# Performance work log

Measured on AMD Instinct MI355X. Metric: run time of the kernel, lower is better.

Reference implementation:

```python
import jax, jax.numpy as jnp
import numpy as np

N, C = 131072, 32          # scene points, raw feature channels
K, L, B1 = 2048, 64, 8     # points per leaf, num leaves, level-1 branching
D_PROJ, D_HID, D = 128, 256, 512


def _lin(key, fan_in, fan_out):
    return jax.random.normal(key, (fan_in, fan_out), jnp.float32) / np.sqrt(fan_in)


def setup_inputs() -> dict:
    key = jax.random.key(0)
    ks = jax.random.split(key, 12)
    coords = jax.random.normal(ks[0], (N, 3), jnp.float32)
    feats = jax.random.normal(ks[1], (N, C), jnp.float32)
    # regular partition of the scene into 64 leaves of 2048 points each
    leaf_indices = jnp.arange(N, dtype=jnp.int32).reshape(L, K)
    leaf_center_idx = jax.random.randint(ks[2], (L,), 0, N, dtype=jnp.int32)
    l1_center_idx = jax.random.randint(ks[3], (B1,), 0, N, dtype=jnp.int32)
    return {
        'coords': coords, 'feats': feats,
        'leaf_indices': leaf_indices,
        'leaf_center_idx': leaf_center_idx,
        'l1_center_idx': l1_center_idx,
        'root_center_idx': 0,
        # projection MLP: C -> 128 -> 128
        'Wp1': _lin(ks[4], C, D_PROJ), 'bp1': jnp.zeros((D_PROJ,), jnp.float32),
        'Wp2': _lin(ks[5], D_PROJ, D_PROJ), 'bp2': jnp.zeros((D_PROJ,), jnp.float32),
        # encoder per-point MLP: (3 + 128) -> 256 -> 512
        'We1': _lin(ks[6], 3 + D_PROJ, D_HID), 'be1': jnp.zeros((D_HID,), jnp.float32),
        'We2': _lin(ks[7], D_HID, D), 'be2': jnp.zeros((D,), jnp.float32),
        # aggregator: (D + 3) -> 512 per child, max-pool, 512 -> 512
        'Wa1': _lin(ks[8], D + 3, D), 'ba1': jnp.zeros((D,), jnp.float32),
        'Wa2': _lin(ks[9], D, D), 'ba2': jnp.zeros((D,), jnp.float32),
    }


def reference(coords, feats, leaf_indices, leaf_center_idx, l1_center_idx,
              root_center_idx, Wp1, bp1, Wp2, bp2, We1, be1, We2, be2,
              Wa1, ba1, Wa2, ba2):
    # ---- leaves: gather + projection + PointNet encoder (batched over all leaves) ----
    pts = coords[leaf_indices]                       # (L, K, 3)
    pf = feats[leaf_indices]                         # (L, K, C)
    centers = coords[leaf_center_idx]                # (L, 3)
    rel = pts - centers[:, None, :]                  # relative coords
    proj = jax.nn.relu(pf @ Wp1 + bp1) @ Wp2 + bp2   # (L, K, D_PROJ)
    x = jnp.concatenate([rel, proj], axis=-1)        # (L, K, 3+D_PROJ)
    h = jax.nn.relu(x @ We1 + be1)                   # (L, K, D_HID)
    point_feats = jax.nn.relu(h @ We2 + be2)         # (L, K, D)
    leaf_feat = point_feats.max(axis=1)              # (L, D) max pool per leaf

    # ---- aggregator with spatial context ----
    def aggregate(child_feats, child_pos, parent_pos):
        r = child_pos - parent_pos[None, :]                       # (M, 3)
        z = jnp.concatenate([child_feats, r], axis=-1)            # (M, D+3)
        g = jax.nn.relu(z @ Wa1 + ba1)                            # (M, D)
        return g.max(axis=0) @ Wa2 + ba2                          # (D,)

    # level 1: each of B1 parents aggregates L//B1 leaf children
    cf = leaf_feat.reshape(B1, L // B1, D)
    cp = centers.reshape(B1, L // B1, 3)
    pp = coords[l1_center_idx]                                    # (B1, 3)
    level1 = jax.vmap(aggregate)(cf, cp, pp)                      # (B1, D)

    # level 0: root aggregates the B1 level-1 features
    root = aggregate(level1, pp, coords[root_center_idx])         # (D,)

    # rows: [level_0 (1), level_1 (B1), level_2 (L)]
    return jnp.concatenate([root[None, :], level1, leaf_feat], axis=0)
```

## Files before the change

kernel.cpp:

```cpp
#include <hip/hip_runtime.h>

#define NPTS   131072
#define CIN    32
#define KPL    2048
#define NLEAF  64
#define NB1    8
#define DPJ    128
#define DHID   256
#define DOUT   512
#define TM     128

typedef __attribute__((ext_vector_type(8))) short  short8;
typedef __attribute__((ext_vector_type(4))) float  f32x4;

__device__ __forceinline__ unsigned short f2bf(float x) {
    unsigned u = __float_as_uint(x);
    u += 0x7FFFu + ((u >> 16) & 1u);
    return (unsigned short)(u >> 16);
}

__global__ __launch_bounds__(256) void convert_weights(
    const float* __restrict__ Wp1, const float* __restrict__ Wp2,
    const float* __restrict__ We1, const float* __restrict__ We2,
    unsigned short* __restrict__ wp1t, unsigned short* __restrict__ wp2t,
    unsigned short* __restrict__ we1t, unsigned short* __restrict__ we2t)
{
    int idx = blockIdx.x * 256 + threadIdx.x;
    if (idx < 4096) {
        int n = idx / 32, k = idx % 32;
        wp1t[idx] = f2bf(Wp1[k * DPJ + n]);
    } else if (idx < 20480) {
        int i = idx - 4096;
        int n = i / 128, k = i % 128;
        wp2t[i] = f2bf(Wp2[k * DPJ + n]);
    } else if (idx < 53248) {
        int i = idx - 20480;
        int n = i / 128, k = i % 128;
        we1t[i] = f2bf(We1[(k + 3) * DHID + n]);
    } else if (idx < 184320) {
        int i = idx - 53248;
        int n = i / 256, k = i % 256;
        we2t[i] = f2bf(We2[k * DOUT + n]);
    }
}

template<int MF, int NF, int KSTEPS, int SB, int WK>
__device__ __forceinline__ void gemm_core(
    const char* sIn, const unsigned short* __restrict__ wt,
    const float* __restrict__ bias, int cb, int lr, int lg, f32x4 acc[MF][NF])
{
    #pragma unroll
    for (int n = 0; n < NF; ++n) {
        float bv = bias[cb + 16 * n + lr];
        #pragma unroll
        for (int m = 0; m < MF; ++m) acc[m][n] = f32x4{bv, bv, bv, bv};
    }
    #pragma unroll
    for (int kk = 0; kk < KSTEPS; ++kk) {
        short8 b[NF];
        #pragma unroll
        for (int n = 0; n < NF; ++n)
            b[n] = *reinterpret_cast<const short8*>(
                wt + (size_t)(cb + 16 * n + lr) * WK + kk * 32 + lg * 8);
        #pragma unroll
        for (int m = 0; m < MF; ++m) {
            int row  = 16 * m + lr;
            int byte = (row * SB + kk * 64 + lg * 16) ^ ((row & 7) << 4);
            short8 a = *reinterpret_cast<const short8*>(sIn + byte);
            #pragma unroll
            for (int n = 0; n < NF; ++n)
                acc[m][n] = __builtin_amdgcn_mfma_f32_16x16x32_bf16(a, b[n], acc[m][n], 0, 0, 0);
        }
    }
}

template<int MF, int NF, int SB, bool RELU>
__device__ __forceinline__ void store_frag(char* sOut, int cb, int lr, int lg, f32x4 acc[MF][NF])
{
    #pragma unroll
    for (int m = 0; m < MF; ++m) {
        #pragma unroll
        for (int r = 0; r < 4; ++r) {
            int row = 16 * m + lg * 4 + r;
            int rb  = row * SB;
            int sw  = (row & 7) << 4;
            #pragma unroll
            for (int n = 0; n < NF; ++n) {
                float v = acc[m][n][r];
                if (RELU) v = fmaxf(v, 0.f);
                int byte = (rb + (cb + 16 * n + lr) * 2) ^ sw;
                *reinterpret_cast<unsigned short*>(sOut + byte) = f2bf(v);
            }
        }
    }
}

template<int MF, int NF>
__device__ __forceinline__ void pool_frag(float* dst, int cb, int lr, int lg, f32x4 acc[MF][NF])
{
    #pragma unroll
    for (int n = 0; n < NF; ++n) {
        float vm = 0.f;
        #pragma unroll
        for (int m = 0; m < MF; ++m) {
            #pragma unroll
            for (int r = 0; r < 4; ++r) vm = fmaxf(vm, acc[m][n][r]);
        }
        vm = fmaxf(vm, __shfl_xor(vm, 16));
        vm = fmaxf(vm, __shfl_xor(vm, 32));
        if (lg == 0)
            atomicMax(reinterpret_cast<int*>(dst + cb + 16 * n + lr),
                      __float_as_int(vm));
    }
}

__global__ __launch_bounds__(256, 1) void leaf_mfma_kernel(
    const float* __restrict__ coords, const float* __restrict__ feats,
    const int* __restrict__ leaf_indices, const int* __restrict__ leaf_center_idx,
    const unsigned short* __restrict__ wp1t, const float* __restrict__ bp1,
    const unsigned short* __restrict__ wp2t, const float* __restrict__ bp2,
    const unsigned short* __restrict__ we1t, const float* __restrict__ be1,
    const float* __restrict__ We1raw,
    const unsigned short* __restrict__ we2t, const float* __restrict__ be2,
    float* __restrict__ leaf_out)
{
    __shared__ __align__(16) char bufH [TM * DHID * 2];
    __shared__ __align__(16) char bufP2[TM * DPJ * 2];
    __shared__ float s_rel[TM][4];
    __shared__ float s_we1rel[3 * DHID];

    const int t    = threadIdx.x;
    const int lane = t & 63;
    const int w    = t >> 6;
    const int lr   = lane & 15;
    const int lg   = lane >> 4;

    const int l     = blockIdx.x >> 4;
    const int chunk = blockIdx.x & 15;
    const int base  = l * KPL + chunk * TM;

    {
        const int p  = t >> 1;
        const int kq = (t & 1) << 4;
        const int gi = leaf_indices[base + p];
        const float* src = feats + (size_t)gi * CIN + kq;
        float4 v0 = *reinterpret_cast<const float4*>(src);
        float4 v1 = *reinterpret_cast<const float4*>(src + 4);
        float4 v2 = *reinterpret_cast<const float4*>(src + 8);
        float4 v3 = *reinterpret_cast<const float4*>(src + 12);
        short8 o0, o1;
        o0[0] = (short)f2bf(v0.x); o0[1] = (short)f2bf(v0.y);
        o0[2] = (short)f2bf(v0.z); o0[3] = (short)f2bf(v0.w);
        o0[4] = (short)f2bf(v1.x); o0[5] = (short)f2bf(v1.y);
        o0[6] = (short)f2bf(v1.z); o0[7] = (short)f2bf(v1.w);
        o1[0] = (short)f2bf(v2.x); o1[1] = (short)f2bf(v2.y);
        o1[2] = (short)f2bf(v2.z); o1[3] = (short)f2bf(v2.w);
        o1[4] = (short)f2bf(v3.x); o1[5] = (short)f2bf(v3.y);
        o1[6] = (short)f2bf(v3.z); o1[7] = (short)f2bf(v3.w);
        const int sw = (p & 7) << 4;
        int b0 = (p * (CIN * 2) + kq * 2) ^ sw;
        int b1 = (p * (CIN * 2) + kq * 2 + 16) ^ sw;
        *reinterpret_cast<short8*>(bufH + b0) = o0;
        *reinterpret_cast<short8*>(bufH + b1) = o1;
    }
    if (t < TM) {
        const int gi = leaf_indices[base + t];
        const int ci = leaf_center_idx[l];
        s_rel[t][0] = coords[gi * 3 + 0] - coords[ci * 3 + 0];
        s_rel[t][1] = coords[gi * 3 + 1] - coords[ci * 3 + 1];
        s_rel[t][2] = coords[gi * 3 + 2] - coords[ci * 3 + 2];
    }
    #pragma unroll
    for (int j = 0; j < 3; ++j) s_we1rel[j * DHID + t] = We1raw[j * DHID + t];
    __syncthreads();

    {
        f32x4 acc[8][2];
        gemm_core<8, 2, 1, CIN * 2, 32>(bufH, wp1t, bp1, w * 32, lr, lg, acc);
        store_frag<8, 2, DPJ * 2, true>(bufH + TM * CIN * 2, w * 32, lr, lg, acc);
    }
    __syncthreads();

    {
        f32x4 acc[8][2];
        gemm_core<8, 2, 4, DPJ * 2, 128>(bufH + TM * CIN * 2, wp2t, bp2, w * 32, lr, lg, acc);
        store_frag<8, 2, DPJ * 2, false>(bufP2, w * 32, lr, lg, acc);
    }
    __syncthreads();

    {
        const int cb = w * 64;
        f32x4 acc[8][4];
        gemm_core<8, 4, 4, DPJ * 2, 128>(bufP2, we1t, be1, cb, lr, lg, acc);
        #pragma unroll
        for (int m = 0; m < 8; ++m) {
            #pragma unroll
            for (int r = 0; r < 4; ++r) {
                int row = 16 * m + lg * 4 + r;
                float r0 = s_rel[row][0], r1 = s_rel[row][1], r2 = s_rel[row][2];
                #pragma unroll
                for (int n = 0; n < 4; ++n) {
                    int col = cb + 16 * n + lr;
                    acc[m][n][r] += r0 * s_we1rel[col]
                                  + r1 * s_we1rel[DHID + col]
                                  + r2 * s_we1rel[2 * DHID + col];
                }
            }
        }
        store_frag<8, 4, DHID * 2, true>(bufH, cb, lr, lg, acc);
    }
    __syncthreads();

    {
        float* const dst = leaf_out + (size_t)l * DOUT;
        #pragma unroll
        for (int p4 = 0; p4 < 2; ++p4) {
            const int cb = w * 128 + p4 * 64;
            f32x4 acc[8][4];
            gemm_core<8, 4, 8, DHID * 2, 256>(bufH, we2t, be2, cb, lr, lg, acc);
            pool_frag<8, 4>(dst, cb, lr, lg, acc);
        }
    }
}

__global__ __launch_bounds__(256) void agg_pool_kernel(
    const float* __restrict__ child,
    const float* __restrict__ coords,
    const int* __restrict__ child_idx,
    const int* __restrict__ parent_idx,
    const float* __restrict__ Wa1, const float* __restrict__ ba1,
    float* __restrict__ pooled)
{
    __shared__ float s_z[NB1][516];
    __shared__ float s_red[4][NB1][64];

    const int t  = threadIdx.x;
    const int b  = blockIdx.x;
    const int p  = b >> 3, cc = b & 7;
    const int c  = t & 63;
    const int col = cc * 64 + c;
    const int ks = t >> 6;

    {
        const int m = t >> 5, tt = t & 31;
        const float* src = child + (size_t)(p * NB1 + m) * DOUT;
        #pragma unroll
        for (int i = 0; i < 4; ++i) {
            const int idx = (i * 32 + tt) * 4;
            *reinterpret_cast<float4*>(&s_z[m][idx]) =
                *reinterpret_cast<const float4*>(src + idx);
        }
    }
    if (t < 24) {
        const int m = t / 3, j = t % 3;
        s_z[m][512 + j] = coords[child_idx[p * NB1 + m] * 3 + j]
                        - coords[parent_idx[p] * 3 + j];
    }
    __syncthreads();

    float acc[NB1] = {0.f, 0.f, 0.f, 0.f, 0.f, 0.f, 0.f, 0.f};
    const int k0 = ks * 128;
    #pragma unroll 32
    for (int i = 0; i < 128; ++i) {
        const int k = k0 + i;
        const float wv = Wa1[(size_t)k * DOUT + col];
        #pragma unroll
        for (int m = 0; m < NB1; ++m) acc[m] += s_z[m][k] * wv;
    }
    if (ks == 3) {
        #pragma unroll
        for (int k = 512; k < 515; ++k) {
            const float wv = Wa1[(size_t)k * DOUT + col];
            #pragma unroll
            for (int m = 0; m < NB1; ++m) acc[m] += s_z[m][k] * wv;
        }
    }
    #pragma unroll
    for (int m = 0; m < NB1; ++m) s_red[ks][m][c] = acc[m];
    __syncthreads();

    if (t < 64) {
        const float bv = ba1[col];
        float pm = 0.f;
        #pragma unroll
        for (int m = 0; m < NB1; ++m) {
            float v = bv + s_red[0][m][c] + s_red[1][m][c]
                         + s_red[2][m][c] + s_red[3][m][c];
            pm = fmaxf(pm, v);
        }
        pooled[(size_t)p * DOUT + col] = pm;
    }
}

__global__ __launch_bounds__(256) void agg_out_kernel(
    const float* __restrict__ pooled,
    const float* __restrict__ Wa2, const float* __restrict__ ba2,
    float* __restrict__ outbase)
{
    __shared__ float s_p[DOUT];
    __shared__ float s_red[4][64];

    const int t  = threadIdx.x;
    const int b  = blockIdx.x;
    const int p  = b >> 3, cc = b & 7;
    const int c  = t & 63;
    const int col = cc * 64 + c;
    const int ks = t >> 6;

    if (t < 128)
        *reinterpret_cast<float4*>(&s_p[t * 4]) =
            *reinterpret_cast<const float4*>(pooled + (size_t)p * DOUT + t * 4);
    __syncthreads();

    float acc = 0.f;
    const int k0 = ks * 128;
    #pragma unroll 32
    for (int i = 0; i < 128; ++i) {
        const int k = k0 + i;
        acc += s_p[k] * Wa2[(size_t)k * DOUT + col];
    }
    s_red[ks][c] = acc;
    __syncthreads();

    if (t < 64)
        outbase[(size_t)p * DOUT + col] =
            ba2[col] + s_red[0][c] + s_red[1][c] + s_red[2][c] + s_red[3][c];
}

extern "C" void kernel_launch(void* const* d_in, const int* in_sizes, int n_in,
                              void* d_out, int out_size, void* d_ws, size_t ws_size,
                              hipStream_t stream)
{
    const float* coords          = (const float*)d_in[0];
    const float* feats           = (const float*)d_in[1];
    const int*   leaf_indices    = (const int*)d_in[2];
    const int*   leaf_center_idx = (const int*)d_in[3];
    const int*   l1_center_idx   = (const int*)d_in[4];
    const int*   root_center_idx = (const int*)d_in[5];
    const float* Wp1 = (const float*)d_in[6];
    const float* bp1 = (const float*)d_in[7];
    const float* Wp2 = (const float*)d_in[8];
    const float* bp2 = (const float*)d_in[9];
    const float* We1 = (const float*)d_in[10];
    const float* be1 = (const float*)d_in[11];
    const float* We2 = (const float*)d_in[12];
    const float* be2 = (const float*)d_in[13];
    const float* Wa1 = (const float*)d_in[14];
    const float* ba1 = (const float*)d_in[15];
    const float* Wa2 = (const float*)d_in[16];
    const float* ba2 = (const float*)d_in[17];

    float* out = (float*)d_out;
    char*  ws  = (char*)d_ws;
    unsigned short* wp1t     = (unsigned short*)ws;
    unsigned short* wp2t     = (unsigned short*)(ws + 8192);
    unsigned short* we1t     = (unsigned short*)(ws + 40960);
    unsigned short* we2t     = (unsigned short*)(ws + 106496);
    float*          pooledL1 = (float*)(ws + 368640);
    float*          pooledR  = (float*)(ws + 385024);

    hipMemsetAsync(out + (size_t)(1 + NB1) * DOUT, 0,
                   (size_t)NLEAF * DOUT * sizeof(float), stream);

    convert_weights<<<dim3(720), dim3(256), 0, stream>>>(
        Wp1, Wp2, We1, We2, wp1t, wp2t, we1t, we2t);

    leaf_mfma_kernel<<<dim3(NLEAF * (KPL / TM)), dim3(256), 0, stream>>>(
        coords, feats, leaf_indices, leaf_center_idx,
        wp1t, bp1, wp2t, bp2, we1t, be1, We1, we2t, be2,
        out + (size_t)(1 + NB1) * DOUT);

    agg_pool_kernel<<<dim3(NB1 * 8), dim3(256), 0, stream>>>(
        out + (size_t)(1 + NB1) * DOUT, coords, leaf_center_idx, l1_center_idx,
        Wa1, ba1, pooledL1);
    agg_out_kernel<<<dim3(NB1 * 8), dim3(256), 0, stream>>>(
        pooledL1, Wa2, ba2, out + DOUT);

    agg_pool_kernel<<<dim3(8), dim3(256), 0, stream>>>(
        out + DOUT, coords, l1_center_idx, root_center_idx,
        Wa1, ba1, pooledR);
    agg_out_kernel<<<dim3(8), dim3(256), 0, stream>>>(
        pooledR, Wa2, ba2, out);
}
```

Baseline: 119.3 us.

## Fold Wp2 into We1 to drop a per-point GEMM in leaf kernel

Because no nonlinearity sits between the second projection layer and the first encoder layer, Wp2·We1[3:] and the matching bias are precomputed once per call by a new fuse_weights kernel. The leaf kernel then runs one 128x256 GEMM on the relu'd projection output instead of a 128x128 GEMM followed by a 128x256 GEMM, removing one GEMM stage and one barrier per tile. The trade-offs are an extra small launch, a change in bf16 rounding order, and a single 96KB shared buffer whose regions are reused across stages.

Result: no change. 119.9 us (+0.5%).

```diff
diff --git a/kernel.cpp b/kernel.cpp
--- a/kernel.cpp
+++ b/kernel.cpp
@@ -20,27 +20,41 @@
 }
 
 __global__ __launch_bounds__(256) void convert_weights(
-    const float* __restrict__ Wp1, const float* __restrict__ Wp2,
-    const float* __restrict__ We1, const float* __restrict__ We2,
-    unsigned short* __restrict__ wp1t, unsigned short* __restrict__ wp2t,
-    unsigned short* __restrict__ we1t, unsigned short* __restrict__ we2t)
+    const float* __restrict__ Wp1, const float* __restrict__ We2,
+    unsigned short* __restrict__ wp1t, unsigned short* __restrict__ we2t)
 {
     int idx = blockIdx.x * 256 + threadIdx.x;
     if (idx < 4096) {
         int n = idx / 32, k = idx % 32;
         wp1t[idx] = f2bf(Wp1[k * DPJ + n]);
-    } else if (idx < 20480) {
+    } else if (idx < 4096 + 131072) {
         int i = idx - 4096;
-        int n = i / 128, k = i % 128;
-        wp2t[i] = f2bf(Wp2[k * DPJ + n]);
-    } else if (idx < 53248) {
-        int i = idx - 20480;
-        int n = i / 128, k = i % 128;
-        we1t[i] = f2bf(We1[(k + 3) * DHID + n]);
-    } else if (idx < 184320) {
-        int i = idx - 53248;
         int n = i / 256, k = i % 256;
         we2t[i] = f2bf(We2[k * DOUT + n]);
+    }
+}
+
+__global__ __launch_bounds__(256) void fuse_weights(
+    const float* __restrict__ Wp2, const float* __restrict__ We1,
+    const float* __restrict__ bp2, const float* __restrict__ be1,
+    unsigned short* __restrict__ wft, float* __restrict__ bfused)
+{
+    int idx = blockIdx.x * 256 + threadIdx.x;
+    int n = idx >> 7;
+    int k = idx & 127;
+    float a0 = 0.f, a1 = 0.f, a2 = 0.f, a3 = 0.f;
+    for (int j = 0; j < DPJ; j += 4) {
+        a0 += Wp2[k * DPJ + j    ] * We1[(3 + j    ) * DHID + n];
+        a1 += Wp2[k * DPJ + j + 1] * We1[(4 + j    ) * DHID + n];
+        a2 += Wp2[k * DPJ + j + 2] * We1[(5 + j    ) * DHID + n];
+        a3 += Wp2[k * DPJ + j + 3] * We1[(6 + j    ) * DHID + n];
+    }
+    wft[n * DPJ + k] = f2bf((a0 + a1) + (a2 + a3));
+    if (idx < DHID) {
+        float b = be1[idx];
+        for (int j = 0; j < DPJ; ++j)
+            b += bp2[j] * We1[(3 + j) * DHID + idx];
+        bfused[idx] = b;
     }
 }
 
@@ -118,14 +132,12 @@
     const float* __restrict__ coords, const float* __restrict__ feats,
     const int* __restrict__ leaf_indices, const int* __restrict__ leaf_center_idx,
     const unsigned short* __restrict__ wp1t, const float* __restrict__ bp1,
-    const unsigned short* __restrict__ wp2t, const float* __restrict__ bp2,
-    const unsigned short* __restrict__ we1t, const float* __restrict__ be1,
+    const unsigned short* __restrict__ wft, const float* __restrict__ bfused,
     const float* __restrict__ We1raw,
     const unsigned short* __restrict__ we2t, const float* __restrict__ be2,
     float* __restrict__ leaf_out)
 {
-    __shared__ __align__(16) char bufH [TM * DHID * 2];
-    __shared__ __align__(16) char bufP2[TM * DPJ * 2];
+    __shared__ __align__(16) char buf[96 * 1024];
     __shared__ float s_rel[TM][4];
     __shared__ float s_we1rel[3 * DHID];
 
@@ -138,6 +150,10 @@
     const int l     = blockIdx.x >> 4;
     const int chunk = blockIdx.x & 15;
     const int base  = l * KPL + chunk * TM;
+
+    char* const sX  = buf;
+    char* const sH  = buf;
+    char* const sP1 = buf + 65536;
 
     {
         const int p  = t >> 1;
@@ -160,8 +176,8 @@
         const int sw = (p & 7) << 4;
         int b0 = (p * (CIN * 2) + kq * 2) ^ sw;
         int b1 = (p * (CIN * 2) + kq * 2 + 16) ^ sw;
-        *reinterpret_cast<short8*>(bufH + b0) = o0;
-        *reinterpret_cast<short8*>(bufH + b1) = o1;
+        *reinterpret_cast<short8*>(sX + b0) = o0;
+        *reinterpret_cast<short8*>(sX + b1) = o1;
     }
     if (t < TM) {
         const int gi = leaf_indices[base + t];
@@ -176,22 +192,15 @@
 
     {
         f32x4 acc[8][2];
-        gemm_core<8, 2, 1, CIN * 2, 32>(bufH, wp1t, bp1, w * 32, lr, lg, acc);
-        store_frag<8, 2, DPJ * 2, true>(bufH + TM * CIN * 2, w * 32, lr, lg, acc);
-    }
-    __syncthreads();
-
-    {
-        f32x4 acc[8][2];
-        gemm_core<8, 2, 4, DPJ * 2, 128>(bufH + TM * CIN * 2, wp2t, bp2, w * 32, lr, lg, acc);
-        store_frag<8, 2, DPJ * 2, false>(bufP2, w * 32, lr, lg, acc);
+        gemm_core<8, 2, 1, CIN * 2, 32>(sX, wp1t, bp1, w * 32, lr, lg, acc);
+        store_frag<8, 2, DPJ * 2, true>(sP1, w * 32, lr, lg, acc);
     }
     __syncthreads();
 
     {
         const int cb = w * 64;
         f32x4 acc[8][4];
-        gemm_core<8, 4, 4, DPJ * 2, 128>(bufP2, we1t, be1, cb, lr, lg, acc);
+        gemm_core<8, 4, 4, DPJ * 2, DPJ>(sP1, wft, bfused, cb, lr, lg, acc);
         #pragma unroll
         for (int m = 0; m < 8; ++m) {
             #pragma unroll
@@ -207,7 +216,7 @@
                 }
             }
         }
-        store_frag<8, 4, DHID * 2, true>(bufH, cb, lr, lg, acc);
+        store_frag<8, 4, DHID * 2, true>(sH, cb, lr, lg, acc);
     }
     __syncthreads();
 
@@ -217,7 +226,7 @@
         for (int p4 = 0; p4 < 2; ++p4) {
             const int cb = w * 128 + p4 * 64;
             f32x4 acc[8][4];
-            gemm_core<8, 4, 8, DHID * 2, 256>(bufH, we2t, be2, cb, lr, lg, acc);
+            gemm_core<8, 4, 8, DHID * 2, 256>(sH, we2t, be2, cb, lr, lg, acc);
             pool_frag<8, 4>(dst, cb, lr, lg, acc);
         }
     }
@@ -353,21 +362,24 @@
     float* out = (float*)d_out;
     char*  ws  = (char*)d_ws;
     unsigned short* wp1t     = (unsigned short*)ws;
-    unsigned short* wp2t     = (unsigned short*)(ws + 8192);
-    unsigned short* we1t     = (unsigned short*)(ws + 40960);
-    unsigned short* we2t     = (unsigned short*)(ws + 106496);
-    float*          pooledL1 = (float*)(ws + 368640);
-    float*          pooledR  = (float*)(ws + 385024);
+    unsigned short* we2t     = (unsigned short*)(ws + 8192);
+    unsigned short* wft      = (unsigned short*)(ws + 270336);
+    float*          bfused   = (float*)(ws + 335872);
+    float*          pooledL1 = (float*)(ws + 336896);
+    float*          pooledR  = (float*)(ws + 353280);
 
     hipMemsetAsync(out + (size_t)(1 + NB1) * DOUT, 0,
                    (size_t)NLEAF * DOUT * sizeof(float), stream);
 
-    convert_weights<<<dim3(720), dim3(256), 0, stream>>>(
-        Wp1, Wp2, We1, We2, wp1t, wp2t, we1t, we2t);
+    convert_weights<<<dim3(528), dim3(256), 0, stream>>>(
+        Wp1, We2, wp1t, we2t);
+
+    fuse_weights<<<dim3(128), dim3(256), 0, stream>>>(
+        Wp2, We1, bp2, be1, wft, bfused);
 
     leaf_mfma_kernel<<<dim3(NLEAF * (KPL / TM)), dim3(256), 0, stream>>>(
         coords, feats, leaf_indices, leaf_center_idx,
-        wp1t, bp1, wp2t, bp2, we1t, be1, We1, we2t, be2,
+        wp1t, bp1, wft, bfused, We1, we2t, be2,
         out + (size_t)(1 + NB1) * DOUT);
 
     agg_pool_kernel<<<dim3(NB1 * 8), dim3(256), 0, stream>>>(
```
